# Kernel tuning notes

Measured on AMD Instinct MI355X. Metric: run time of the kernel, lower is better.

## Reference

```python
import jax, jax.numpy as jnp
import numpy as np

D = 1024
H = 16
T_BLOCK = 2048


def setup_inputs() -> dict:
    key = jax.random.key(0)
    ks = jax.random.split(key, 12)
    B, T = 2, 2048
    s = lambda k, shape: jax.random.normal(k, shape, jnp.float32) * 0.02
    return {
        "x": jax.random.normal(ks[0], (B, T, D), jnp.float32),
        # layernorms
        "ln1_g": jnp.ones((D,), jnp.float32), "ln1_b": jnp.zeros((D,), jnp.float32),
        "ln2_g": jnp.ones((D,), jnp.float32), "ln2_b": jnp.zeros((D,), jnp.float32),
        # attention qkv projection ([in,out] layout) and output proj
        "w_qkv": s(ks[1], (D, 3 * D)), "b_qkv": jnp.zeros((3 * D,), jnp.float32),
        "w_o": s(ks[2], (D, D)), "b_o": jnp.zeros((D,), jnp.float32),
        # MLP
        "w_fc1": s(ks[3], (D, 4 * D)), "b_fc1": jnp.zeros((4 * D,), jnp.float32),
        "w_fc2": s(ks[4], (4 * D, D)), "b_fc2": jnp.zeros((D,), jnp.float32),
    }


def _layernorm(x, g, b, eps=1e-5):
    mu = jnp.mean(x, axis=-1, keepdims=True)
    var = jnp.var(x, axis=-1, keepdims=True)
    return (x - mu) * jax.lax.rsqrt(var + eps) * g + b


def _attention(x, w_qkv, b_qkv, w_o, b_o):
    B, T, C = x.shape
    hd = C // H
    qkv = x @ w_qkv + b_qkv                      # [B,T,3C]
    q, k, v = jnp.split(qkv, 3, axis=-1)
    split = lambda t: t.reshape(B, T, H, hd).transpose(0, 2, 1, 3)  # [B,H,T,hd]
    q, k, v = split(q), split(k), split(v)
    att = jnp.einsum("bhqd,bhkd->bhqk", q, k) / jnp.sqrt(jnp.float32(hd))
    causal = jnp.tril(jnp.ones((T, T), bool))
    att = jnp.where(causal[None, None], att, -jnp.inf)
    att = jax.nn.softmax(att, axis=-1)
    y = jnp.einsum("bhqk,bhkd->bhqd", att, v)    # [B,H,T,hd]
    y = y.transpose(0, 2, 1, 3).reshape(B, T, C)
    return y @ w_o + b_o


def reference(x, ln1_g, ln1_b, ln2_g, ln2_b, w_qkv, b_qkv, w_o, b_o,
              w_fc1, b_fc1, w_fc2, b_fc2):
    # dropout is identity in eval mode
    x = x + _attention(_layernorm(x, ln1_g, ln1_b), w_qkv, b_qkv, w_o, b_o)
    h = jax.nn.gelu(_layernorm(x, ln2_g, ln2_b) @ w_fc1 + b_fc1)
    return x + (h @ w_fc2 + b_fc2)
```

## Files before the change

### kernel.cpp

```cpp
#include <hip/hip_runtime.h>
#include <hip/hip_bf16.h>


using bf16 = __bf16;
using bf16x8 = __attribute__((ext_vector_type(8))) __bf16;
using floatx4 = __attribute__((ext_vector_type(4))) float;

#define D_ 1024
#define T_ 2048
#define B_ 2
#define H_ 16

static __device__ __forceinline__ bf16 f2bf(float f) { return (bf16)f; }

static __device__ __forceinline__ void async16(const void* g, void* l) {
  __builtin_amdgcn_global_load_lds(
      (const __attribute__((address_space(1))) void*)g,
      (__attribute__((address_space(3))) void*)l, 16, 0, 0);
}

static __device__ __forceinline__ float gelu_f(float v) {
  const float u2 = 1.5957691216057308f * (v + 0.044715f * v * v * v);
  return v / (1.0f + __expf(-u2));
}

__global__ void transpose_cast(const float* __restrict__ in, bf16* __restrict__ out,
                               int K, int N) {
  __shared__ float tile[32][33];
  const int n0 = blockIdx.x * 32, k0 = blockIdx.y * 32;
  const int tx = threadIdx.x, ty = threadIdx.y;
  for (int i = 0; i < 32; i += 8)
    tile[ty + i][tx] = in[(size_t)(k0 + ty + i) * N + n0 + tx];
  __syncthreads();
  for (int i = 0; i < 32; i += 8)
    out[(size_t)(n0 + ty + i) * K + k0 + tx] = f2bf(tile[tx][ty + i]);
}

__global__ __launch_bounds__(256)
void ln_kernel(const float* __restrict__ x, const float* __restrict__ g,
               const float* __restrict__ bsh, bf16* __restrict__ out) {
  const int row = blockIdx.x, tid = threadIdx.x;
  const float4 v = ((const float4*)(x + (size_t)row * D_))[tid];
  float s = v.x + v.y + v.z + v.w;
  float s2 = v.x * v.x + v.y * v.y + v.z * v.z + v.w * v.w;
  for (int off = 32; off; off >>= 1) {
    s += __shfl_xor(s, off);
    s2 += __shfl_xor(s2, off);
  }
  __shared__ float red[8];
  const int wave = tid >> 6, lane = tid & 63;
  if (lane == 0) { red[wave] = s; red[wave + 4] = s2; }
  __syncthreads();
  s = red[0] + red[1] + red[2] + red[3];
  s2 = red[4] + red[5] + red[6] + red[7];
  const float mu = s * (1.0f / D_);
  const float rstd = rsqrtf(s2 * (1.0f / D_) - mu * mu + 1e-5f);
  const float4 gv = ((const float4*)g)[tid];
  const float4 bv = ((const float4*)bsh)[tid];
  bf16 o[4] __attribute__((aligned(8)));
  o[0] = f2bf((v.x - mu) * rstd * gv.x + bv.x);
  o[1] = f2bf((v.y - mu) * rstd * gv.y + bv.y);
  o[2] = f2bf((v.z - mu) * rstd * gv.z + bv.z);
  o[3] = f2bf((v.w - mu) * rstd * gv.w + bv.w);
  *(ushort4*)(out + (size_t)row * D_ + tid * 4) = *(const ushort4*)o;
}

template <int EPI>
__global__ __launch_bounds__(256)
void gemm_bt(const bf16* __restrict__ A, const bf16* __restrict__ Bt,
             const float* __restrict__ bias, const float* __restrict__ res,
             void* __restrict__ Cout, int M, int N, int K) {
  __shared__ __align__(16) bf16 As[128][64];
  __shared__ __align__(16) bf16 Bs[128][64];
  const int tid = threadIdx.x;
  const int wave = tid >> 6, lane = tid & 63;
  const int quad = lane >> 4, l16 = lane & 15;
  const int wr = wave >> 1, wc = wave & 1;
  const int bm = blockIdx.x * 128, bn = blockIdx.y * 128;
  const int lrow8 = lane >> 3;
  const int lcol = (((lane & 7) ^ lrow8) * 8);

  floatx4 acc[4][4] = {};

  for (int k0 = 0; k0 < K; k0 += 64) {
    __syncthreads();
    for (int c = 0; c < 4; c++) {
      const int r = wave * 32 + c * 8;
      async16(&A[(size_t)(bm + r + lrow8) * K + k0 + lcol], &As[r][0]);
      async16(&Bt[(size_t)(bn + r + lrow8) * K + k0 + lcol], &Bs[r][0]);
    }
    __syncthreads();
    for (int ks = 0; ks < 2; ks++) {
      const int fc = ((quad + ks * 4) ^ (l16 & 7)) * 8;
      bf16x8 af[4], bfr[4];
      for (int mt = 0; mt < 4; mt++)
        af[mt] = *(const bf16x8*)&As[wr * 64 + mt * 16 + l16][fc];
      for (int nt = 0; nt < 4; nt++)
        bfr[nt] = *(const bf16x8*)&Bs[wc * 64 + nt * 16 + l16][fc];
      for (int mt = 0; mt < 4; mt++)
        for (int nt = 0; nt < 4; nt++)
          acc[mt][nt] = __builtin_amdgcn_mfma_f32_16x16x32_bf16(
              af[mt], bfr[nt], acc[mt][nt], 0, 0, 0);
    }
  }

  for (int mt = 0; mt < 4; mt++) {
    for (int nt = 0; nt < 4; nt++) {
      const int col = bn + wc * 64 + nt * 16 + l16;
      const float bcol = bias[col];
      for (int i = 0; i < 4; i++) {
        const int row = bm + wr * 64 + mt * 16 + quad * 4 + i;
        float v = acc[mt][nt][i] + bcol;
        if (EPI == 0) {
          ((bf16*)Cout)[(size_t)row * N + col] = f2bf(v);
        } else if (EPI == 1) {
          ((bf16*)Cout)[(size_t)row * N + col] = f2bf(gelu_f(v));
        } else {
          ((float*)Cout)[(size_t)row * N + col] = v + res[(size_t)row * N + col];
        }
      }
    }
  }
}

template <int EPI>
__global__ __launch_bounds__(256)
void gemm64_k128(const bf16* __restrict__ A, const bf16* __restrict__ Bt,
                 const float* __restrict__ bias, const float* __restrict__ res,
                 void* __restrict__ Cout, int M, int N, int K) {
  __shared__ __align__(16) bf16 As[64][128];
  __shared__ __align__(16) bf16 Bs[128][128];
  const int tid = threadIdx.x;
  const int wave = tid >> 6, lane = tid & 63;
  const int quad = lane >> 4, l16 = lane & 15;
  const int wr = wave >> 1, wc = wave & 1;
  const int bm = blockIdx.x * 64, bn = blockIdx.y * 128;
  const int sr = lane >> 4;
  const int pchunk = lane & 15;

  floatx4 acc[2][4] = {};

  for (int k0 = 0; k0 < K; k0 += 128) {
    __syncthreads();
    for (int c = 0; c < 4; c++) {
      const int base = wave * 16 + c * 4;
      const int scol = (pchunk ^ ((c * 4 + sr) & 15)) * 8;
      async16(&A[(size_t)(bm + base + sr) * K + k0 + scol], &As[base][0]);
    }
    for (int c = 0; c < 8; c++) {
      const int base = wave * 32 + c * 4;
      const int scol = (pchunk ^ ((c * 4 + sr) & 15)) * 8;
      async16(&Bt[(size_t)(bn + base + sr) * K + k0 + scol], &Bs[base][0]);
    }
    __syncthreads();
    for (int ks = 0; ks < 4; ks++) {
      const int fc = ((quad + ks * 4) ^ l16) * 8;
      bf16x8 af[2], bfr[4];
      for (int mt = 0; mt < 2; mt++)
        af[mt] = *(const bf16x8*)&As[wr * 32 + mt * 16 + l16][fc];
      for (int nt = 0; nt < 4; nt++)
        bfr[nt] = *(const bf16x8*)&Bs[wc * 64 + nt * 16 + l16][fc];
      for (int mt = 0; mt < 2; mt++)
        for (int nt = 0; nt < 4; nt++)
          acc[mt][nt] = __builtin_amdgcn_mfma_f32_16x16x32_bf16(
              af[mt], bfr[nt], acc[mt][nt], 0, 0, 0);
    }
  }

  for (int mt = 0; mt < 2; mt++) {
    for (int nt = 0; nt < 4; nt++) {
      const int col = bn + wc * 64 + nt * 16 + l16;
      const float bcol = bias[col];
      for (int i = 0; i < 4; i++) {
        const int row = bm + wr * 32 + mt * 16 + quad * 4 + i;
        float v = acc[mt][nt][i] + bcol;
        if (EPI == 0) {
          ((bf16*)Cout)[(size_t)row * N + col] = f2bf(v);
        } else if (EPI == 1) {
          ((bf16*)Cout)[(size_t)row * N + col] = f2bf(gelu_f(v));
        } else {
          ((float*)Cout)[(size_t)row * N + col] = v + res[(size_t)row * N + col];
        }
      }
    }
  }
}

__global__ __launch_bounds__(256)
void attn_kernel(const bf16* __restrict__ qkv, bf16* __restrict__ y) {
  const int bh = blockIdx.y, b = bh >> 4, h = bh & 15;
  const int tile = (blockIdx.y & 16) ? (int)blockIdx.x : (15 - (int)blockIdx.x);
  const int q0 = tile * 128;
  const int tid = threadIdx.x, wave = tid >> 6, lane = tid & 63;
  const int quad = lane >> 4, l16 = lane & 15;
  const int w32 = wave * 32;

  constexpr int PAD = 80;
  __shared__ __align__(16) bf16 Ks[64][PAD];
  __shared__ __align__(16) bf16 Vts[64][PAD];
  __shared__ __align__(16) bf16 Ps[128][PAD];

  const size_t bbase = (size_t)b * T_ * 3072 + (size_t)h * 64;
  const bf16* Qg = qkv + bbase;
  const bf16* Kg = qkv + bbase + 1024;
  const bf16* Vg = qkv + bbase + 2048;

  bf16x8 ones;
  for (int j = 0; j < 8; j++) ones[j] = f2bf(1.0f);

  const int kr0 = tid >> 3, kc0 = (tid & 7) * 8;
  const int kr1 = (tid + 256) >> 3;

  bf16x8 qf[2][2];
  for (int mt = 0; mt < 2; mt++)
    for (int ks = 0; ks < 2; ks++) {
      bf16x8 t = *(const bf16x8*)
          &Qg[(size_t)(q0 + w32 + mt * 16 + l16) * 3072 + ks * 32 + quad * 8];
      for (int j = 0; j < 8; j++) t[j] = f2bf((float)t[j] * 0.125f);
      qf[mt][ks] = t;
    }

  int4 kreg0 = *(const int4*)&Kg[(size_t)kr0 * 3072 + kc0];
  int4 kreg1 = *(const int4*)&Kg[(size_t)kr1 * 3072 + kc0];
  bf16x8 vreg[2];
  for (int i = 0; i < 2; i++)
    vreg[i] = *(const bf16x8*)&Vg[(size_t)lane * 3072 + (wave + i * 4) * 8];

  floatx4 accY[2][4] = {};
  floatx4 accL[2] = {};

  const int kend = q0 + 64;
  for (int kc = 0; kc <= kend; kc += 64) {
    __syncthreads();
    *(int4*)&Ks[kr0][kc0] = kreg0;
    *(int4*)&Ks[kr1][kc0] = kreg1;
    for (int i = 0; i < 2; i++) {
      const int dc = wave + i * 4;
      for (int j = 0; j < 8; j++) Vts[dc * 8 + j][lane] = vreg[i][j];
    }
    __syncthreads();

    if (kc < kend) {
      kreg0 = *(const int4*)&Kg[(size_t)(kc + 64 + kr0) * 3072 + kc0];
      kreg1 = *(const int4*)&Kg[(size_t)(kc + 64 + kr1) * 3072 + kc0];
      for (int i = 0; i < 2; i++)
        vreg[i] = *(const bf16x8*)
            &Vg[(size_t)(kc + 64 + lane) * 3072 + (wave + i * 4) * 8];
    }

    floatx4 s[2][4];
    for (int nt = 0; nt < 4; nt++) {
      bf16x8 kf0 = *(const bf16x8*)&Ks[nt * 16 + l16][quad * 8];
      bf16x8 kf1 = *(const bf16x8*)&Ks[nt * 16 + l16][32 + quad * 8];
      for (int mt = 0; mt < 2; mt++) {
        floatx4 t = {};
        t = __builtin_amdgcn_mfma_f32_16x16x32_bf16(qf[mt][0], kf0, t, 0, 0, 0);
        t = __builtin_amdgcn_mfma_f32_16x16x32_bf16(qf[mt][1], kf1, t, 0, 0, 0);
        s[mt][nt] = t;
      }
    }
    for (int mt = 0; mt < 2; mt++)
      if (kc + 64 > q0 + w32 + mt * 16) {
        for (int nt = 0; nt < 4; nt++)
          for (int i = 0; i < 4; i++) {
            const int c = kc + nt * 16 + l16;
            const int r = q0 + w32 + mt * 16 + quad * 4 + i;
            if (c > r) s[mt][nt][i] = -1e30f;
          }
      }

    for (int mt = 0; mt < 2; mt++)
      for (int i = 0; i < 4; i++) {
        bf16* prow = &Ps[w32 + mt * 16 + quad * 4 + i][l16];
        for (int nt = 0; nt < 4; nt++)
          prow[nt * 16] = f2bf(__expf(s[mt][nt][i] - 8.0f));
      }
    __builtin_amdgcn_wave_barrier();

    for (int mt = 0; mt < 2; mt++) {
      for (int ks = 0; ks < 2; ks++) {
        bf16x8 pa = *(const bf16x8*)&Ps[w32 + mt * 16 + l16][ks * 32 + quad * 8];
        for (int dt = 0; dt < 4; dt++) {
          bf16x8 vb = *(const bf16x8*)&Vts[dt * 16 + l16][ks * 32 + quad * 8];
          accY[mt][dt] =
              __builtin_amdgcn_mfma_f32_16x16x32_bf16(pa, vb, accY[mt][dt], 0, 0, 0);
        }
        accL[mt] = __builtin_amdgcn_mfma_f32_16x16x32_bf16(pa, ones, accL[mt], 0, 0, 0);
      }
    }
  }

  for (int mt = 0; mt < 2; mt++)
    for (int i = 0; i < 4; i++) {
      const float linv = 1.0f / accL[mt][i];
      const int r = q0 + w32 + mt * 16 + quad * 4 + i;
      for (int dt = 0; dt < 4; dt++)
        y[(size_t)(b * T_ + r) * D_ + h * 64 + dt * 16 + l16] =
            f2bf(accY[mt][dt][i] * linv);
    }
}

extern "C" void kernel_launch(void* const* d_in, const int* in_sizes, int n_in,
                              void* d_out, int out_size, void* d_ws, size_t ws_size,
                              hipStream_t stream) {
  const float* x     = (const float*)d_in[0];
  const float* ln1_g = (const float*)d_in[1];
  const float* ln1_b = (const float*)d_in[2];
  const float* ln2_g = (const float*)d_in[3];
  const float* ln2_b = (const float*)d_in[4];
  const float* w_qkv = (const float*)d_in[5];
  const float* b_qkv = (const float*)d_in[6];
  const float* w_o   = (const float*)d_in[7];
  const float* b_o   = (const float*)d_in[8];
  const float* w_fc1 = (const float*)d_in[9];
  const float* b_fc1 = (const float*)d_in[10];
  const float* w_fc2 = (const float*)d_in[11];
  const float* b_fc2 = (const float*)d_in[12];

  char* p = (char*)d_ws;
  bf16* wqkvT = (bf16*)p; p += (size_t)3072 * 1024 * 2;
  bf16* woT   = (bf16*)p; p += (size_t)1024 * 1024 * 2;
  bf16* wfc1T = (bf16*)p; p += (size_t)4096 * 1024 * 2;
  bf16* wfc2T = (bf16*)p; p += (size_t)1024 * 4096 * 2;
  bf16* ln1   = (bf16*)p; p += (size_t)4096 * 1024 * 2;
  bf16* qkv   = (bf16*)p; p += (size_t)4096 * 3072 * 2;
  bf16* yb    = (bf16*)p; p += (size_t)4096 * 1024 * 2;
  float* x2   = (float*)p; p += (size_t)4096 * 1024 * 4;
  bf16* ln2   = (bf16*)p; p += (size_t)4096 * 1024 * 2;
  bf16* hb    = (bf16*)p; p += (size_t)4096 * 4096 * 2;

  const dim3 tb(32, 8);
  transpose_cast<<<dim3(96, 32), tb, 0, stream>>>(w_qkv, wqkvT, 1024, 3072);
  transpose_cast<<<dim3(32, 32), tb, 0, stream>>>(w_o, woT, 1024, 1024);
  transpose_cast<<<dim3(128, 32), tb, 0, stream>>>(w_fc1, wfc1T, 1024, 4096);
  transpose_cast<<<dim3(32, 128), tb, 0, stream>>>(w_fc2, wfc2T, 4096, 1024);

  ln_kernel<<<4096, 256, 0, stream>>>(x, ln1_g, ln1_b, ln1);
  gemm_bt<0><<<dim3(32, 24), 256, 0, stream>>>(ln1, wqkvT, b_qkv, nullptr, qkv,
                                               4096, 3072, 1024);
  attn_kernel<<<dim3(16, 32), 256, 0, stream>>>(qkv, yb);
  gemm64_k128<2><<<dim3(64, 8), 256, 0, stream>>>(yb, woT, b_o, x, x2,
                                                  4096, 1024, 1024);
  ln_kernel<<<4096, 256, 0, stream>>>(x2, ln2_g, ln2_b, ln2);
  gemm_bt<1><<<dim3(32, 32), 256, 0, stream>>>(ln2, wfc1T, b_fc1, nullptr, hb,
                                               4096, 4096, 1024);
  gemm64_k128<2><<<dim3(64, 8), 256, 0, stream>>>(hb, wfc2T, b_fc2, x2, (float*)d_out,
                                                  4096, 1024, 4096);
}
```

Before: 331.1 us.

## Use 8 waves of 16 query rows in attention with XOR-swizzled LDS

The attention kernel now runs 512 threads as 8 waves, each handling 16 query rows instead of 32. This halves the per-wave register state and gives more waves to hide latency per block. The padded LDS tiles for K, transposed V and P are replaced by unpadded 64-column tiles with an XOR swizzle on 8-element chunks, which avoids bank conflicts while using less LDS. In exchange, each K/V tile is amortised over fewer rows per wave, and the extra waves add barrier and scheduling overhead.

```diff
diff --git a/kernel.cpp b/kernel.cpp
--- a/kernel.cpp
+++ b/kernel.cpp
@@ -186,19 +186,19 @@
   }
 }
 
-__global__ __launch_bounds__(256)
+__global__ __launch_bounds__(512)
 void attn_kernel(const bf16* __restrict__ qkv, bf16* __restrict__ y) {
   const int bh = blockIdx.y, b = bh >> 4, h = bh & 15;
   const int tile = (blockIdx.y & 16) ? (int)blockIdx.x : (15 - (int)blockIdx.x);
   const int q0 = tile * 128;
   const int tid = threadIdx.x, wave = tid >> 6, lane = tid & 63;
   const int quad = lane >> 4, l16 = lane & 15;
-  const int w32 = wave * 32;
-
-  constexpr int PAD = 80;
-  __shared__ __align__(16) bf16 Ks[64][PAD];
-  __shared__ __align__(16) bf16 Vts[64][PAD];
-  __shared__ __align__(16) bf16 Ps[128][PAD];
+  const int l7 = l16 & 7;
+  const int w16 = wave * 16;
+
+  __shared__ __align__(16) bf16 Ks[64][64];
+  __shared__ __align__(16) bf16 Vts[64][64];
+  __shared__ __align__(16) bf16 Ps[128][64];
 
   const size_t bbase = (size_t)b * T_ * 3072 + (size_t)h * 64;
   const bf16* Qg = qkv + bbase;
@@ -208,96 +208,85 @@
   bf16x8 ones;
   for (int j = 0; j < 8; j++) ones[j] = f2bf(1.0f);
 
-  const int kr0 = tid >> 3, kc0 = (tid & 7) * 8;
-  const int kr1 = (tid + 256) >> 3;
-
-  bf16x8 qf[2][2];
-  for (int mt = 0; mt < 2; mt++)
-    for (int ks = 0; ks < 2; ks++) {
-      bf16x8 t = *(const bf16x8*)
-          &Qg[(size_t)(q0 + w32 + mt * 16 + l16) * 3072 + ks * 32 + quad * 8];
-      for (int j = 0; j < 8; j++) t[j] = f2bf((float)t[j] * 0.125f);
-      qf[mt][ks] = t;
-    }
-
-  int4 kreg0 = *(const int4*)&Kg[(size_t)kr0 * 3072 + kc0];
-  int4 kreg1 = *(const int4*)&Kg[(size_t)kr1 * 3072 + kc0];
-  bf16x8 vreg[2];
-  for (int i = 0; i < 2; i++)
-    vreg[i] = *(const bf16x8*)&Vg[(size_t)lane * 3072 + (wave + i * 4) * 8];
-
-  floatx4 accY[2][4] = {};
-  floatx4 accL[2] = {};
+  const int kr = tid >> 3, kch = tid & 7;
+  const int kcol = ((kch ^ (kr & 7)) * 8);
+  const int vk = tid & 63, vd = tid >> 6;
+
+  bf16x8 qf[2];
+  for (int ks = 0; ks < 2; ks++) {
+    bf16x8 t = *(const bf16x8*)
+        &Qg[(size_t)(q0 + w16 + l16) * 3072 + ks * 32 + quad * 8];
+    for (int j = 0; j < 8; j++) t[j] = f2bf((float)t[j] * 0.125f);
+    qf[ks] = t;
+  }
+
+  int4 kreg = *(const int4*)&Kg[(size_t)kr * 3072 + kch * 8];
+  bf16x8 vreg = *(const bf16x8*)&Vg[(size_t)vk * 3072 + vd * 8];
+
+  floatx4 accY[4] = {};
+  floatx4 accL = {};
 
   const int kend = q0 + 64;
   for (int kc = 0; kc <= kend; kc += 64) {
     __syncthreads();
-    *(int4*)&Ks[kr0][kc0] = kreg0;
-    *(int4*)&Ks[kr1][kc0] = kreg1;
-    for (int i = 0; i < 2; i++) {
-      const int dc = wave + i * 4;
-      for (int j = 0; j < 8; j++) Vts[dc * 8 + j][lane] = vreg[i][j];
+    *(int4*)&Ks[kr][kcol] = kreg;
+    for (int j = 0; j < 8; j++) {
+      const int d = vd * 8 + j;
+      Vts[d][((vk >> 3) ^ j) * 8 + (vk & 7)] = vreg[j];
     }
     __syncthreads();
 
     if (kc < kend) {
-      kreg0 = *(const int4*)&Kg[(size_t)(kc + 64 + kr0) * 3072 + kc0];
-      kreg1 = *(const int4*)&Kg[(size_t)(kc + 64 + kr1) * 3072 + kc0];
-      for (int i = 0; i < 2; i++)
-        vreg[i] = *(const bf16x8*)
-            &Vg[(size_t)(kc + 64 + lane) * 3072 + (wave + i * 4) * 8];
-    }
-
-    floatx4 s[2][4];
+      kreg = *(const int4*)&Kg[(size_t)(kc + 64 + kr) * 3072 + kch * 8];
+      vreg = *(const bf16x8*)&Vg[(size_t)(kc + 64 + vk) * 3072 + vd * 8];
+    }
+
+    floatx4 s[4];
     for (int nt = 0; nt < 4; nt++) {
-      bf16x8 kf0 = *(const bf16x8*)&Ks[nt * 16 + l16][quad * 8];
-      bf16x8 kf1 = *(const bf16x8*)&Ks[nt * 16 + l16][32 + quad * 8];
-      for (int mt = 0; mt < 2; mt++) {
-        floatx4 t = {};
-        t = __builtin_amdgcn_mfma_f32_16x16x32_bf16(qf[mt][0], kf0, t, 0, 0, 0);
-        t = __builtin_amdgcn_mfma_f32_16x16x32_bf16(qf[mt][1], kf1, t, 0, 0, 0);
-        s[mt][nt] = t;
+      const bf16* krow = &Ks[nt * 16 + l16][0];
+      bf16x8 kf0 = *(const bf16x8*)&krow[(quad ^ l7) * 8];
+      bf16x8 kf1 = *(const bf16x8*)&krow[((4 + quad) ^ l7) * 8];
+      floatx4 t = {};
+      t = __builtin_amdgcn_mfma_f32_16x16x32_bf16(qf[0], kf0, t, 0, 0, 0);
+      t = __builtin_amdgcn_mfma_f32_16x16x32_bf16(qf[1], kf1, t, 0, 0, 0);
+      s[nt] = t;
+    }
+    if (kc + 64 > q0 + w16) {
+      for (int nt = 0; nt < 4; nt++)
+        for (int i = 0; i < 4; i++) {
+          const int c = kc + nt * 16 + l16;
+          const int r = q0 + w16 + quad * 4 + i;
+          if (c > r) s[nt][i] = -1e30f;
+        }
+    }
+
+    for (int i = 0; i < 4; i++) {
+      const int pr = quad * 4 + i;
+      bf16* prow = &Ps[w16 + pr][0];
+      for (int nt = 0; nt < 4; nt++)
+        prow[(((nt * 2 + (l16 >> 3)) ^ (pr & 7)) * 8) + l7] =
+            f2bf(__expf(s[nt][i] - 8.0f));
+    }
+    __builtin_amdgcn_wave_barrier();
+
+    for (int ks = 0; ks < 2; ks++) {
+      bf16x8 pa = *(const bf16x8*)&Ps[w16 + l16][((ks * 4 + quad) ^ l7) * 8];
+      for (int dt = 0; dt < 4; dt++) {
+        bf16x8 vb = *(const bf16x8*)&Vts[dt * 16 + l16][((ks * 4 + quad) ^ l7) * 8];
+        accY[dt] =
+            __builtin_amdgcn_mfma_f32_16x16x32_bf16(pa, vb, accY[dt], 0, 0, 0);
       }
-    }
-    for (int mt = 0; mt < 2; mt++)
-      if (kc + 64 > q0 + w32 + mt * 16) {
-        for (int nt = 0; nt < 4; nt++)
-          for (int i = 0; i < 4; i++) {
-            const int c = kc + nt * 16 + l16;
-            const int r = q0 + w32 + mt * 16 + quad * 4 + i;
-            if (c > r) s[mt][nt][i] = -1e30f;
-          }
-      }
-
-    for (int mt = 0; mt < 2; mt++)
-      for (int i = 0; i < 4; i++) {
-        bf16* prow = &Ps[w32 + mt * 16 + quad * 4 + i][l16];
-        for (int nt = 0; nt < 4; nt++)
-          prow[nt * 16] = f2bf(__expf(s[mt][nt][i] - 8.0f));
-      }
-    __builtin_amdgcn_wave_barrier();
-
-    for (int mt = 0; mt < 2; mt++) {
-      for (int ks = 0; ks < 2; ks++) {
-        bf16x8 pa = *(const bf16x8*)&Ps[w32 + mt * 16 + l16][ks * 32 + quad * 8];
-        for (int dt = 0; dt < 4; dt++) {
-          bf16x8 vb = *(const bf16x8*)&Vts[dt * 16 + l16][ks * 32 + quad * 8];
-          accY[mt][dt] =
-              __builtin_amdgcn_mfma_f32_16x16x32_bf16(pa, vb, accY[mt][dt], 0, 0, 0);
-        }
-        accL[mt] = __builtin_amdgcn_mfma_f32_16x16x32_bf16(pa, ones, accL[mt], 0, 0, 0);
-      }
-    }
-  }
-
-  for (int mt = 0; mt < 2; mt++)
-    for (int i = 0; i < 4; i++) {
-      const float linv = 1.0f / accL[mt][i];
-      const int r = q0 + w32 + mt * 16 + quad * 4 + i;
-      for (int dt = 0; dt < 4; dt++)
-        y[(size_t)(b * T_ + r) * D_ + h * 64 + dt * 16 + l16] =
-            f2bf(accY[mt][dt][i] * linv);
-    }
+      accL = __builtin_amdgcn_mfma_f32_16x16x32_bf16(pa, ones, accL, 0, 0, 0);
+    }
+  }
+
+  for (int i = 0; i < 4; i++) {
+    const float linv = 1.0f / accL[i];
+    const int r = q0 + w16 + quad * 4 + i;
+    for (int dt = 0; dt < 4; dt++)
+      y[(size_t)(b * T_ + r) * D_ + h * 64 + dt * 16 + l16] =
+          f2bf(accY[dt][i] * linv);
+  }
 }
 
 extern "C" void kernel_launch(void* const* d_in, const int* in_sizes, int n_in,
@@ -338,7 +327,7 @@
   ln_kernel<<<4096, 256, 0, stream>>>(x, ln1_g, ln1_b, ln1);
   gemm_bt<0><<<dim3(32, 24), 256, 0, stream>>>(ln1, wqkvT, b_qkv, nullptr, qkv,
                                                4096, 3072, 1024);
-  attn_kernel<<<dim3(16, 32), 256, 0, stream>>>(qkv, yb);
+  attn_kernel<<<dim3(16, 32), 512, 0, stream>>>(qkv, yb);
   gemm64_k128<2><<<dim3(64, 8), 256, 0, stream>>>(yb, woT, b_o, x, x2,
                                                   4096, 1024, 1024);
   ln_kernel<<<4096, 256, 0, stream>>>(x2, ln2_g, ln2_b, ln2);
```

After: 319.0 us. 1.04x faster.
